# Optimization experiments

Hardware: AMD Instinct MI355X
Metric: run time of the kernel (lower is better)

## Reference

```python
import jax, jax.numpy as jnp
import numpy as np

HID = 512       # hidden_dim (embed/LSTM input)
HDE = 512       # hidden_dim_de == attn_channels (required by conv_att channel count)
NCLS = 7000
LSEQ = 40
B = 128
FH, FW = 8, 32


def setup_inputs() -> dict:
    key = jax.random.key(0)
    ks = jax.random.split(key, 16)
    s = 0.05
    inp = {
        "hidden_en": jax.random.normal(ks[0], (1, B, HID), jnp.float32),
        "x_em": jax.random.normal(ks[1], (B, HDE, FH, FW), jnp.float32),
        "att_x_em": jax.random.normal(ks[2], (B, FH * FW, HDE), jnp.float32),
        "target": jax.random.randint(ks[3], (B, LSEQ), 0, NCLS),
        "feature_h": FH,
        "feature_w": FW,
        # parameters
        "embed_w": jax.random.normal(ks[4], (NCLS, HID), jnp.float32) * s,
        "W_ih": jax.random.normal(ks[5], (4 * HDE, HID), jnp.float32) * s,   # LSTMCell input weights (i,f,g,o)
        "W_hh": jax.random.normal(ks[6], (4 * HDE, HDE), jnp.float32) * s,
        "b_ih": jax.random.normal(ks[7], (4 * HDE,), jnp.float32) * s,
        "b_hh": jax.random.normal(ks[8], (4 * HDE,), jnp.float32) * s,
        "hem_w": jax.random.normal(ks[9], (HDE, HDE), jnp.float32) * s,     # 1x1 conv h_em as matrix
        "hem_b": jax.random.normal(ks[10], (HDE,), jnp.float32) * s,
        "attw_w": jax.random.normal(ks[11], (HDE,), jnp.float32) * s,       # 1x1 conv conv_att -> 1 channel
        "attw_b": jax.random.normal(ks[12], (), jnp.float32) * s,
        "lin_w": jax.random.normal(ks[13], (NCLS, HDE + HDE), jnp.float32) * s,
        "lin_b": jax.random.normal(ks[14], (NCLS,), jnp.float32) * s,
    }
    return inp


def _decode(hidden_en, x_em, att_x_em, target, embed_w, W_ih, W_hh, b_ih, b_hh,
            hem_w, hem_b, attw_w, attw_b, lin_w, lin_b):
    L = target.shape[1]
    # teacher-forced inputs: step 0 uses hidden_en[-1], step t>=1 uses embed(target[:, t-1])
    xt0 = hidden_en[-1]                                   # [B, HID]
    xts = jnp.concatenate([xt0[None], jnp.transpose(embed_w[target[:, : L - 1]], (1, 0, 2))], axis=0)  # [L,B,HID]
    xg_all = jnp.einsum('lbi,gi->lbg', xts, W_ih) + b_ih  # precompute input gates [L,B,4H]
    Bn = x_em.shape[0]
    h0 = jnp.zeros((Bn, HDE), x_em.dtype)
    c0 = jnp.zeros((Bn, HDE), x_em.dtype)

    def step(carry, xg):
        h, c = carry
        gates = xg + h @ W_hh.T + b_hh
        i, f, g, o = jnp.split(gates, 4, axis=-1)
        c = jax.nn.sigmoid(f) * c + jax.nn.sigmoid(i) * jnp.tanh(g)
        h = jax.nn.sigmoid(o) * jnp.tanh(c)
        # additive attention (dropout treated as identity for determinism)
        hem = h @ hem_w.T + hem_b                          # [B, C]
        feat = jnp.tanh(x_em + hem[:, :, None, None])      # [B, C, H, W]
        feat_att = jnp.einsum('bchw,c->bhw', feat, attw_w) + attw_b
        alpha = jax.nn.softmax(feat_att.reshape(Bn, -1), axis=-1)  # [B, HW]
        att = jnp.einsum('bn,bnd->bd', alpha, att_x_em)    # [B, C]
        scores = jax.nn.log_softmax(jnp.concatenate([h, att], -1) @ lin_w.T + lin_b)
        return (h, c), scores

    _, ys = jax.lax.scan(step, (h0, c0), xg_all)           # ys: [L, B, NCLS]
    return jnp.transpose(ys, (1, 0, 2))                    # [B, L, NCLS]


def reference(hidden_en, x_em, att_x_em, target, feature_h, feature_w,
              embed_w, W_ih, W_hh, b_ih, b_hh, hem_w, hem_b, attw_w, attw_b,
              lin_w, lin_b):
    return _decode(hidden_en, x_em, att_x_em, target, embed_w, W_ih, W_hh,
                   b_ih, b_hh, hem_w, hem_b, attw_w, attw_b, lin_w, lin_b)
```

## Files before the change

kernel.cpp:

```cpp
#include <hip/hip_runtime.h>

#define B_    128
#define HIDD  512
#define NCLS  7000
#define NPAD  7040
#define LSEQ  40
#define MROWS 5120
#define TT    10
#define SBLK  16

typedef __attribute__((ext_vector_type(8))) short bf16x8;
typedef __attribute__((ext_vector_type(4))) float f32x4;

__device__ __forceinline__ unsigned short f2bf(float x) {
  union { float f; unsigned u; } v; v.f = x;
  unsigned r = v.u + 0x7fffu + ((v.u >> 16) & 1u);
  return (unsigned short)(r >> 16);
}
__device__ __forceinline__ float bf2f(unsigned short h) {
  union { unsigned u; float f; } v; v.u = ((unsigned)h) << 16;
  return v.f;
}
__device__ __forceinline__ float sigm(float x) { return 1.f / (1.f + __expf(-x)); }
__device__ __forceinline__ float tanh_f(float x) {
  float e = __expf(2.f * x);
  return 1.f - 2.f / (e + 1.f);
}
__device__ __forceinline__ float rcp_f(float x) { return __builtin_amdgcn_rcpf(x); }

__device__ __forceinline__ void gl_lds16(const void* g, void* l) {
  auto gp = reinterpret_cast<const __attribute__((address_space(1))) unsigned int*>(
      reinterpret_cast<unsigned long long>(g));
  auto lp = reinterpret_cast<__attribute__((address_space(3))) unsigned int*>(
      reinterpret_cast<unsigned long long>(l));
  __builtin_amdgcn_global_load_lds(gp, lp, 16, 0, 0);
}

__global__ __launch_bounds__(256) void k_cvt(const float* __restrict__ src,
                                             unsigned short* __restrict__ dst, int n4) {
  int i = blockIdx.x * 256 + threadIdx.x;
  if (i >= n4) return;
  float4 v = ((const float4*)src)[i];
  ushort4 o; o.x = f2bf(v.x); o.y = f2bf(v.y); o.z = f2bf(v.z); o.w = f2bf(v.w);
  ((ushort4*)dst)[i] = o;
}

__global__ __launch_bounds__(256) void k_cvtp(const float* __restrict__ src,
                                              unsigned short* __restrict__ dst,
                                              const float* __restrict__ b1,
                                              const float* __restrict__ b2,
                                              float* __restrict__ bsum) {
  int i = blockIdx.x * 256 + threadIdx.x;
  int e = i * 4;
  int n = e >> 9, col = e & 511;
  int srow = ((n >> 4) & 3) * 512 + (n >> 6) * 16 + (n & 15);
  float4 v = *(const float4*)(src + (size_t)srow * 512 + col);
  ushort4 o; o.x = f2bf(v.x); o.y = f2bf(v.y); o.z = f2bf(v.z); o.w = f2bf(v.w);
  ((ushort4*)dst)[i] = o;
  if (bsum != nullptr && col == 0) bsum[n] = b1[srow] + b2[srow];
}

__global__ __launch_bounds__(256) void k_expcvt(const float* __restrict__ src,
                                                unsigned short* __restrict__ dst, int n4) {
  int i = blockIdx.x * 256 + threadIdx.x;
  if (i >= n4) return;
  float4 v = ((const float4*)src)[i];
  ushort4 o;
  o.x = f2bf(__expf(2.f * v.x)); o.y = f2bf(__expf(2.f * v.y));
  o.z = f2bf(__expf(2.f * v.z)); o.w = f2bf(__expf(2.f * v.w));
  ((ushort4*)dst)[i] = o;
}

__global__ __launch_bounds__(256) void k_linpad(const float* __restrict__ lw,
                                                unsigned short* __restrict__ dst) {
  int i = blockIdx.x * 256 + threadIdx.x;
  int e = i * 4;
  int row = e >> 10;
  ushort4 o;
  if (row < NCLS) {
    float4 v = *(const float4*)(lw + (size_t)row * 1024 + (e & 1023));
    o.x = f2bf(v.x); o.y = f2bf(v.y); o.z = f2bf(v.z); o.w = f2bf(v.w);
  } else { o.x = 0; o.y = 0; o.z = 0; o.w = 0; }
  ((ushort4*)dst)[i] = o;
}

__global__ __launch_bounds__(256) void k_xts(const float* __restrict__ hidden_en,
                                             const float* __restrict__ embed_w,
                                             const int* __restrict__ target,
                                             unsigned short* __restrict__ xts,
                                             int* __restrict__ cnt) {
  if (blockIdx.x == 0 && threadIdx.x == 0)
    __hip_atomic_store(cnt, 0, __ATOMIC_RELAXED, __HIP_MEMORY_SCOPE_AGENT);
  int i = blockIdx.x * 256 + threadIdx.x;
  int e = i * 4;
  int r = e >> 9, col = e & 511;
  int l = r >> 7, b = r & 127;
  const float* src;
  if (l == 0) src = hidden_en + b * 512 + col;
  else        src = embed_w + (size_t)target[b * LSEQ + (l - 1)] * 512 + col;
  float4 v = *(const float4*)src;
  ushort4 o; o.x = f2bf(v.x); o.y = f2bf(v.y); o.z = f2bf(v.z); o.w = f2bf(v.w);
  ((ushort4*)xts)[i] = o;
}

template <int MODE>
__global__ __launch_bounds__(256) void k_gemm(const unsigned short* __restrict__ A, int lda,
                                              const unsigned short* __restrict__ Bw, int ldb,
                                              const float* __restrict__ bias,
                                              void* __restrict__ outp, int ldc, int K) {
  __shared__ __align__(16) unsigned short As[128 * 32];
  __shared__ __align__(16) unsigned short Bs[128 * 32];
  const int tid = threadIdx.x;
  const int lane = tid & 63, wid = tid >> 6;
  const int wm = wid >> 1, wn = wid & 1;
  const int quad = lane >> 4, l16 = lane & 15;
  const int gr = lane >> 2, gc = (lane & 3) * 8;
  const int m0 = blockIdx.x * 128, n0 = blockIdx.y * 128;
  f32x4 acc[4][4];
#pragma unroll
  for (int i = 0; i < 4; i++)
#pragma unroll
    for (int j = 0; j < 4; j++) acc[i][j] = (f32x4){0.f, 0.f, 0.f, 0.f};

  for (int k0 = 0; k0 < K; k0 += 32) {
#pragma unroll
    for (int s = 0; s < 2; s++) {
      const int rb = s * 64 + wid * 16;
      gl_lds16(A + (size_t)(m0 + rb + gr) * lda + k0 + gc, As + rb * 32);
      gl_lds16(Bw + (size_t)(n0 + rb + gr) * ldb + k0 + gc, Bs + rb * 32);
    }
    __syncthreads();
    bf16x8 af[4], bfr[4];
#pragma unroll
    for (int i = 0; i < 4; i++)
      af[i] = *(const bf16x8*)(As + (wm * 64 + i * 16 + l16) * 32 + quad * 8);
#pragma unroll
    for (int j = 0; j < 4; j++)
      bfr[j] = *(const bf16x8*)(Bs + (wn * 64 + j * 16 + l16) * 32 + quad * 8);
#pragma unroll
    for (int i = 0; i < 4; i++)
#pragma unroll
      for (int j = 0; j < 4; j++)
        acc[i][j] = __builtin_amdgcn_mfma_f32_16x16x32_bf16(af[i], bfr[j], acc[i][j], 0, 0, 0);
    __syncthreads();
  }
#pragma unroll
  for (int i = 0; i < 4; i++) {
    int mbase = m0 + wm * 64 + i * 16 + quad * 4;
#pragma unroll
    for (int j = 0; j < 4; j++) {
      int n = n0 + wn * 64 + j * 16 + l16;
#pragma unroll
      for (int r = 0; r < 4; r++) {
        float v = acc[i][j][r];
        int m = mbase + r;
        if (MODE == 0) {
          ((unsigned short*)outp)[(size_t)m * ldc + n] = f2bf(v + bias[n]);
        } else if (MODE == 3) {
          ((float*)outp)[(size_t)m * ldc + n] = __expf(2.f * (v + bias[n]));
        } else {
          if (n < NCLS) {
            int t = m >> 7, b = m & 127;
            ((float*)outp)[((size_t)(b * LSEQ + t)) * NCLS + n] = v + bias[n];
          }
        }
      }
    }
  }
}

__global__ __launch_bounds__(256) void k_step(const unsigned short* __restrict__ h_prev,
                                              unsigned short* __restrict__ h_new,
                                              float* __restrict__ c_buf,
                                              const unsigned short* __restrict__ xg,
                                              const unsigned short* __restrict__ whhp,
                                              unsigned short* __restrict__ hatt, int t) {
  __shared__ __align__(16) unsigned short As[128 * 32];
  __shared__ __align__(16) unsigned short Bs[128 * 32];
  const int tid = threadIdx.x;
  const int lane = tid & 63, wid = tid >> 6;
  const int wm = wid >> 1, wn = wid & 1;
  const int quad = lane >> 4, l16 = lane & 15;
  const int n0 = blockIdx.x * 128;
  f32x4 acc[4][4];
#pragma unroll
  for (int i = 0; i < 4; i++)
#pragma unroll
    for (int j = 0; j < 4; j++) acc[i][j] = (f32x4){0.f, 0.f, 0.f, 0.f};

  if (t > 0) {
    const int r0 = tid >> 2, kq0 = (tid & 3) * 8;
    for (int k0 = 0; k0 < 512; k0 += 32) {
#pragma unroll
      for (int s = 0; s < 2; s++) {
        int row = r0 + s * 64;
        *(bf16x8*)(As + row * 32 + kq0) = *(const bf16x8*)(h_prev + (size_t)row * 512 + k0 + kq0);
        *(bf16x8*)(Bs + row * 32 + kq0) = *(const bf16x8*)(whhp + (size_t)(n0 + row) * 512 + k0 + kq0);
      }
      __syncthreads();
      bf16x8 af[4], bfr[4];
#pragma unroll
      for (int i = 0; i < 4; i++)
        af[i] = *(const bf16x8*)(As + (wm * 64 + i * 16 + l16) * 32 + quad * 8);
#pragma unroll
      for (int j = 0; j < 4; j++)
        bfr[j] = *(const bf16x8*)(Bs + (wn * 64 + j * 16 + l16) * 32 + quad * 8);
#pragma unroll
      for (int i = 0; i < 4; i++)
#pragma unroll
        for (int j = 0; j < 4; j++)
          acc[i][j] = __builtin_amdgcn_mfma_f32_16x16x32_bf16(af[i], bfr[j], acc[i][j], 0, 0, 0);
      __syncthreads();
    }
  }
  const int jcol = ((n0 >> 6) + wn) * 16 + l16;
#pragma unroll
  for (int i = 0; i < 4; i++) {
    int mbase = wm * 64 + i * 16 + quad * 4;
#pragma unroll
    for (int r = 0; r < 4; r++) {
      int m = mbase + r;
      const unsigned short* xrow = xg + (size_t)(t * 128 + m) * 2048 + n0 + wn * 64 + l16;
      float ip = acc[i][0][r] + bf2f(xrow[0]);
      float fp = acc[i][1][r] + bf2f(xrow[16]);
      float gp = acc[i][2][r] + bf2f(xrow[32]);
      float op = acc[i][3][r] + bf2f(xrow[48]);
      float c_old = (t > 0) ? c_buf[m * 512 + jcol] : 0.f;
      float c = sigm(fp) * c_old + sigm(ip) * tanh_f(gp);
      c_buf[m * 512 + jcol] = c;
      float h = sigm(op) * tanh_f(c);
      unsigned short hb = f2bf(h);
      h_new[m * 512 + jcol] = hb;
      hatt[(size_t)(t * 128 + m) * 1024 + jcol] = hb;
    }
  }
}

__global__ __launch_bounds__(256) void k_scan3(unsigned short* __restrict__ h0,
                                               unsigned short* __restrict__ h1,
                                               const unsigned short* __restrict__ xg,
                                               const unsigned short* __restrict__ whhp,
                                               unsigned short* __restrict__ hatt,
                                               int* __restrict__ cnt) {
  __shared__ __align__(16) unsigned short Wl[128 * 512];
  const int tid = threadIdx.x;
  const int lane = tid & 63, wid = tid >> 6;
  const int wm = wid >> 1, wn = wid & 1;
  const int quad = lane >> 4, l16 = lane & 15;
  const int n0 = blockIdx.x * 128;

  for (int i = tid; i < 128 * 64; i += 256) {
    int row = i >> 6, c8 = (i & 63) << 3;
    bf16x8 v = *(const bf16x8*)(whhp + (size_t)(n0 + row) * 512 + c8);
    *(bf16x8*)((char*)Wl + ((row * 1024 + c8 * 2) ^ ((row & 7) << 4))) = v;
  }
  float cst[4][4];
#pragma unroll
  for (int i = 0; i < 4; i++)
#pragma unroll
    for (int r = 0; r < 4; r++) cst[i][r] = 0.f;
  const int jcol = ((n0 >> 6) + wn) * 16 + l16;
  __syncthreads();

  for (int t = 0; t < LSEQ; t++) {
    f32x4 acc[4][4];
#pragma unroll
    for (int i = 0; i < 4; i++)
#pragma unroll
      for (int j = 0; j < 4; j++) acc[i][j] = (f32x4){0.f, 0.f, 0.f, 0.f};
    if (t > 0) {
      const unsigned short* hp = (t & 1) ? h0 : h1;
      const unsigned short* hb = hp + (size_t)(wm * 64 + l16) * 512 + quad * 8;
#pragma unroll 4
      for (int k0 = 0; k0 < 512; k0 += 32) {
        bf16x8 af[4], bfr[4];
#pragma unroll
        for (int i = 0; i < 4; i++)
          af[i] = *(const bf16x8*)(hb + (size_t)i * 16 * 512 + k0);
#pragma unroll
        for (int j = 0; j < 4; j++) {
          int rw = wn * 64 + j * 16 + l16;
          bfr[j] = *(const bf16x8*)((const char*)Wl +
                    ((rw * 1024 + (k0 + quad * 8) * 2) ^ ((rw & 7) << 4)));
        }
#pragma unroll
        for (int i = 0; i < 4; i++)
#pragma unroll
          for (int j = 0; j < 4; j++)
            acc[i][j] = __builtin_amdgcn_mfma_f32_16x16x32_bf16(af[i], bfr[j], acc[i][j], 0, 0, 0);
      }
    }
    unsigned short* hn = (t & 1) ? h1 : h0;
    const unsigned short* xq = xg + (size_t)(t * 128) * 2048 + n0 + wn * 64 + l16;
#pragma unroll
    for (int i = 0; i < 4; i++) {
#pragma unroll
      for (int r = 0; r < 4; r++) {
        int m = wm * 64 + i * 16 + quad * 4 + r;
        const unsigned short* xrow = xq + (size_t)m * 2048;
        float ip = acc[i][0][r] + bf2f(xrow[0]);
        float fp = acc[i][1][r] + bf2f(xrow[16]);
        float gp = acc[i][2][r] + bf2f(xrow[32]);
        float op = acc[i][3][r] + bf2f(xrow[48]);
        float c = sigm(fp) * cst[i][r] + sigm(ip) * tanh_f(gp);
        cst[i][r] = c;
        float h = sigm(op) * tanh_f(c);
        unsigned short hbv = f2bf(h);
        hn[m * 512 + jcol] = hbv;
        hatt[(size_t)(t * 128 + m) * 1024 + jcol] = hbv;
      }
    }
    if (t < LSEQ - 1) {
      __threadfence();
      __syncthreads();
      if (tid == 0) {
        __hip_atomic_fetch_add(cnt, 1, __ATOMIC_RELEASE, __HIP_MEMORY_SCOPE_AGENT);
        const int tgt = SBLK * (t + 1);
        while (__hip_atomic_load(cnt, __ATOMIC_ACQUIRE, __HIP_MEMORY_SCOPE_AGENT) < tgt)
          __builtin_amdgcn_s_sleep(8);
      }
      __syncthreads();
      __threadfence();
    }
  }
}

__global__ __launch_bounds__(256) void k_feat(const float* __restrict__ Eh,
                                              const unsigned short* __restrict__ Ex,
                                              const float* __restrict__ attw_w,
                                              float* __restrict__ s_all) {
  __shared__ float EhL[TT][512];
  __shared__ float wL[512];
  const int tid = threadIdx.x;
  const int tg = blockIdx.x >> 7, b = blockIdx.x & 127;
  const int t0 = tg * TT;
  for (int i = tid * 4; i < TT * 512; i += 1024) {
    int t = i >> 9, c = i & 511;
    *(float4*)&EhL[t][c] = *(const float4*)&Eh[((size_t)(t0 + t) * 128 + b) * 512 + c];
  }
  if (tid < 128) *(float4*)&wL[tid * 4] = *(const float4*)&attw_w[tid * 4];
  __syncthreads();
  const int p = tid;
  const unsigned short* xp = Ex + (size_t)b * 512 * 256 + p;
  float acc[TT];
#pragma unroll
  for (int t = 0; t < TT; t++) acc[t] = 0.f;
  for (int c0 = 0; c0 < 512; c0 += 4) {
    float ex0 = bf2f(xp[(size_t)(c0 + 0) * 256]);
    float ex1 = bf2f(xp[(size_t)(c0 + 1) * 256]);
    float ex2 = bf2f(xp[(size_t)(c0 + 2) * 256]);
    float ex3 = bf2f(xp[(size_t)(c0 + 3) * 256]);
    float4 wv = *(const float4*)&wL[c0];
#pragma unroll
    for (int t = 0; t < TT; t++) {
      float4 eh = *(const float4*)&EhL[t][c0];
      acc[t] = __builtin_fmaf(wv.x, rcp_f(__builtin_fmaf(ex0, eh.x, 1.f)), acc[t]);
      acc[t] = __builtin_fmaf(wv.y, rcp_f(__builtin_fmaf(ex1, eh.y, 1.f)), acc[t]);
      acc[t] = __builtin_fmaf(wv.z, rcp_f(__builtin_fmaf(ex2, eh.z, 1.f)), acc[t]);
      acc[t] = __builtin_fmaf(wv.w, rcp_f(__builtin_fmaf(ex3, eh.w, 1.f)), acc[t]);
    }
  }
#pragma unroll
  for (int t = 0; t < TT; t++)
    s_all[((size_t)(t0 + t) * 128 + b) * 256 + p] = -2.f * acc[t];
}

__global__ __launch_bounds__(256) void k_att(const float* __restrict__ s_all,
                                             const float* __restrict__ atx,
                                             unsigned short* __restrict__ hatt) {
  __shared__ float sL[40][257];
  __shared__ float zinv[40];
  const int tid = threadIdx.x;
  const int b = blockIdx.x >> 1, dh = blockIdx.x & 1;
  for (int i = tid; i < 40 * 256; i += 256) {
    int t = i >> 8, p = i & 255;
    sL[t][p] = s_all[((size_t)t * 128 + b) * 256 + p];
  }
  __syncthreads();
  if (tid < 40) {
    int t = tid;
    float mx = -1e30f;
    for (int p = 0; p < 256; p++) mx = fmaxf(mx, sL[t][p]);
    float z = 0.f;
    for (int p = 0; p < 256; p++) { float e = __expf(sL[t][p] - mx); sL[t][p] = e; z += e; }
    zinv[t] = 1.f / z;
  }
  __syncthreads();
  float acc[40];
#pragma unroll
  for (int t = 0; t < 40; t++) acc[t] = 0.f;
  const int d = dh * 256 + tid;
  const float* ap = atx + (size_t)b * 256 * 512 + d;
  for (int p = 0; p < 256; p++) {
    float av = ap[(size_t)p * 512];
#pragma unroll
    for (int t = 0; t < 40; t++) acc[t] += sL[t][p] * av;
  }
#pragma unroll
  for (int t = 0; t < 40; t++) {
    float v = acc[t] * zinv[t];
    hatt[((size_t)t * 128 + b) * 1024 + 512 + d] = f2bf(v);
  }
}

__global__ __launch_bounds__(256) void k_lsm(float* __restrict__ out) {
  __shared__ float buf[7000];
  __shared__ float red[256];
  const int tid = threadIdx.x;
  float* pr = out + (size_t)blockIdx.x * NCLS;
  for (int i = tid * 4; i < NCLS; i += 1024)
    *(float4*)&buf[i] = *(const float4*)&pr[i];
  __syncthreads();
  float mx = -1e30f;
  for (int i = tid; i < NCLS; i += 256) mx = fmaxf(mx, buf[i]);
  red[tid] = mx; __syncthreads();
  for (int s = 128; s > 0; s >>= 1) { if (tid < s) red[tid] = fmaxf(red[tid], red[tid + s]); __syncthreads(); }
  mx = red[0]; __syncthreads();
  float sum = 0.f;
  for (int i = tid; i < NCLS; i += 256) sum += __expf(buf[i] - mx);
  red[tid] = sum; __syncthreads();
  for (int s = 128; s > 0; s >>= 1) { if (tid < s) red[tid] += red[tid + s]; __syncthreads(); }
  float lse = mx + __logf(red[0]);
  for (int i = tid * 4; i < NCLS; i += 1024) {
    float4 v = *(const float4*)&buf[i];
    v.x -= lse; v.y -= lse; v.z -= lse; v.w -= lse;
    *(float4*)&pr[i] = v;
  }
}

extern "C" void kernel_launch(void* const* d_in, const int* in_sizes, int n_in,
                              void* d_out, int out_size, void* d_ws, size_t ws_size,
                              hipStream_t stream) {
  const float* hidden_en = (const float*)d_in[0];
  const float* x_em      = (const float*)d_in[1];
  const float* att_x     = (const float*)d_in[2];
  const int*   target    = (const int*)d_in[3];
  const float* embed_w   = (const float*)d_in[6];
  const float* W_ih      = (const float*)d_in[7];
  const float* W_hh      = (const float*)d_in[8];
  const float* b_ih      = (const float*)d_in[9];
  const float* b_hh      = (const float*)d_in[10];
  const float* hem_w     = (const float*)d_in[11];
  const float* hem_b     = (const float*)d_in[12];
  const float* attw_w    = (const float*)d_in[13];
  const float* lin_w     = (const float*)d_in[15];
  const float* lin_b     = (const float*)d_in[16];
  float* out = (float*)d_out;
  (void)in_sizes; (void)n_in; (void)out_size; (void)ws_size;

  char* w = (char*)d_ws;
  size_t off = 0;
  auto alloc = [&](size_t bytes) { char* p = w + off; off = (off + bytes + 255) & ~(size_t)255; return p; };
  unsigned short* xts  = (unsigned short*)alloc((size_t)MROWS * 512 * 2);
  unsigned short* wihp = (unsigned short*)alloc((size_t)2048 * 512 * 2);
  unsigned short* whhp = (unsigned short*)alloc((size_t)2048 * 512 * 2);
  unsigned short* xg   = (unsigned short*)alloc((size_t)MROWS * 2048 * 2);
  unsigned short* hemw = (unsigned short*)alloc((size_t)512 * 512 * 2);
  unsigned short* linw = (unsigned short*)alloc((size_t)NPAD * 1024 * 2);
  unsigned short* xem  = (unsigned short*)alloc((size_t)128 * 512 * 256 * 2);
  unsigned short* hatt = (unsigned short*)alloc((size_t)MROWS * 1024 * 2);
  unsigned short* h0   = (unsigned short*)alloc((size_t)128 * 512 * 2);
  unsigned short* h1   = (unsigned short*)alloc((size_t)128 * 512 * 2);
  float* cb      = (float*)alloc((size_t)128 * 512 * 4);
  float* bsum    = (float*)alloc((size_t)2048 * 4);
  float* eh_all  = (float*)alloc((size_t)MROWS * 512 * 4);
  float* s_all   = (float*)alloc((size_t)MROWS * 256 * 4);
  int*   cnt     = (int*)alloc(256);

  k_cvtp<<<1024, 256, 0, stream>>>(W_ih, wihp, b_ih, b_hh, bsum);
  k_cvtp<<<1024, 256, 0, stream>>>(W_hh, whhp, nullptr, nullptr, nullptr);
  k_cvt<<<256, 256, 0, stream>>>(hem_w, hemw, 512 * 512 / 4);
  k_expcvt<<<16384, 256, 0, stream>>>(x_em, xem, 128 * 512 * 256 / 4);
  k_linpad<<<NPAD * 1024 / 4 / 256, 256, 0, stream>>>(lin_w, linw);
  k_xts<<<MROWS * 512 / 4 / 256, 256, 0, stream>>>(hidden_en, embed_w, target, xts, cnt);
  k_gemm<0><<<dim3(40, 16), 256, 0, stream>>>(xts, 512, wihp, 512, bsum, xg, 2048, 512);

  {
    void* args[] = { (void*)&h0, (void*)&h1, (void*)&xg, (void*)&whhp, (void*)&hatt, (void*)&cnt };
    hipError_t ce = hipLaunchCooperativeKernel(k_scan3, dim3(SBLK), dim3(256), args, 0u, stream);
    if (ce != hipSuccess) {
      for (int t = 0; t < LSEQ; t++) {
        const unsigned short* hp = (t & 1) ? h0 : h1;
        unsigned short* hn = (t & 1) ? h1 : h0;
        k_step<<<16, 256, 0, stream>>>(hp, hn, cb, xg, whhp, hatt, t);
      }
    }
  }

  k_gemm<3><<<dim3(40, 4), 256, 0, stream>>>(hatt, 1024, hemw, 512, hem_b, eh_all, 512, 512);
  k_feat<<<512, 256, 0, stream>>>(eh_all, xem, attw_w, s_all);
  k_att<<<256, 256, 0, stream>>>(s_all, att_x, hatt);

  k_gemm<2><<<dim3(40, 55), 256, 0, stream>>>(hatt, 1024, linw, 1024, lin_b, out, NCLS, 1024);
  k_lsm<<<MROWS, 256, 0, stream>>>(out);
}
```

Baseline: 1.408 ms.

## Fuse preprocessing kernels, relax scan barrier fences, use plain LDS staging in GEMM

Merges six conversion and gather kernels into one launch, which removes several kernel-launch gaps. In the cooperative LSTM scan, the hidden state is now written with cache-bypassing stores and read with nontemporal loads. The thread fences and acquire/release atomics around the grid barrier become relaxed atomics with a shorter sleep, cutting per-step sync cost. The GEMM drops direct global-to-LDS loads in favour of ordinary register-staged copies. Relaxing the memory ordering risks stale h reads if the cache-bypass assumptions do not hold.

```diff
diff --git a/kernel.cpp b/kernel.cpp
--- a/kernel.cpp
+++ b/kernel.cpp
@@ -28,79 +28,73 @@
 }
 __device__ __forceinline__ float rcp_f(float x) { return __builtin_amdgcn_rcpf(x); }
 
-__device__ __forceinline__ void gl_lds16(const void* g, void* l) {
-  auto gp = reinterpret_cast<const __attribute__((address_space(1))) unsigned int*>(
-      reinterpret_cast<unsigned long long>(g));
-  auto lp = reinterpret_cast<__attribute__((address_space(3))) unsigned int*>(
-      reinterpret_cast<unsigned long long>(l));
-  __builtin_amdgcn_global_load_lds(gp, lp, 16, 0, 0);
-}
-
-__global__ __launch_bounds__(256) void k_cvt(const float* __restrict__ src,
-                                             unsigned short* __restrict__ dst, int n4) {
-  int i = blockIdx.x * 256 + threadIdx.x;
-  if (i >= n4) return;
-  float4 v = ((const float4*)src)[i];
-  ushort4 o; o.x = f2bf(v.x); o.y = f2bf(v.y); o.z = f2bf(v.z); o.w = f2bf(v.w);
-  ((ushort4*)dst)[i] = o;
-}
-
-__global__ __launch_bounds__(256) void k_cvtp(const float* __restrict__ src,
-                                              unsigned short* __restrict__ dst,
-                                              const float* __restrict__ b1,
-                                              const float* __restrict__ b2,
-                                              float* __restrict__ bsum) {
-  int i = blockIdx.x * 256 + threadIdx.x;
-  int e = i * 4;
-  int n = e >> 9, col = e & 511;
-  int srow = ((n >> 4) & 3) * 512 + (n >> 6) * 16 + (n & 15);
-  float4 v = *(const float4*)(src + (size_t)srow * 512 + col);
-  ushort4 o; o.x = f2bf(v.x); o.y = f2bf(v.y); o.z = f2bf(v.z); o.w = f2bf(v.w);
-  ((ushort4*)dst)[i] = o;
-  if (bsum != nullptr && col == 0) bsum[n] = b1[srow] + b2[srow];
-}
-
-__global__ __launch_bounds__(256) void k_expcvt(const float* __restrict__ src,
-                                                unsigned short* __restrict__ dst, int n4) {
-  int i = blockIdx.x * 256 + threadIdx.x;
-  if (i >= n4) return;
-  float4 v = ((const float4*)src)[i];
-  ushort4 o;
-  o.x = f2bf(__expf(2.f * v.x)); o.y = f2bf(__expf(2.f * v.y));
-  o.z = f2bf(__expf(2.f * v.z)); o.w = f2bf(__expf(2.f * v.w));
-  ((ushort4*)dst)[i] = o;
-}
-
-__global__ __launch_bounds__(256) void k_linpad(const float* __restrict__ lw,
-                                                unsigned short* __restrict__ dst) {
-  int i = blockIdx.x * 256 + threadIdx.x;
-  int e = i * 4;
-  int row = e >> 10;
-  ushort4 o;
-  if (row < NCLS) {
-    float4 v = *(const float4*)(lw + (size_t)row * 1024 + (e & 1023));
-    o.x = f2bf(v.x); o.y = f2bf(v.y); o.z = f2bf(v.z); o.w = f2bf(v.w);
-  } else { o.x = 0; o.y = 0; o.z = 0; o.w = 0; }
-  ((ushort4*)dst)[i] = o;
-}
-
-__global__ __launch_bounds__(256) void k_xts(const float* __restrict__ hidden_en,
+__global__ __launch_bounds__(256) void k_pre(const float* __restrict__ W_ih,
+                                             const float* __restrict__ W_hh,
+                                             unsigned short* __restrict__ wihp,
+                                             unsigned short* __restrict__ whhp,
+                                             const float* __restrict__ b_ih,
+                                             const float* __restrict__ b_hh,
+                                             float* __restrict__ bsum,
+                                             const float* __restrict__ hem_w,
+                                             unsigned short* __restrict__ hemw,
+                                             const float* __restrict__ x_em,
+                                             unsigned short* __restrict__ xem,
+                                             const float* __restrict__ lin_w,
+                                             unsigned short* __restrict__ linw,
+                                             const float* __restrict__ hidden_en,
                                              const float* __restrict__ embed_w,
                                              const int* __restrict__ target,
                                              unsigned short* __restrict__ xts,
                                              int* __restrict__ cnt) {
-  if (blockIdx.x == 0 && threadIdx.x == 0)
+  const int bid = blockIdx.x, tid = threadIdx.x;
+  if (bid == 0 && tid == 0)
     __hip_atomic_store(cnt, 0, __ATOMIC_RELAXED, __HIP_MEMORY_SCOPE_AGENT);
-  int i = blockIdx.x * 256 + threadIdx.x;
-  int e = i * 4;
-  int r = e >> 9, col = e & 511;
-  int l = r >> 7, b = r & 127;
-  const float* src;
-  if (l == 0) src = hidden_en + b * 512 + col;
-  else        src = embed_w + (size_t)target[b * LSEQ + (l - 1)] * 512 + col;
-  float4 v = *(const float4*)src;
-  ushort4 o; o.x = f2bf(v.x); o.y = f2bf(v.y); o.z = f2bf(v.z); o.w = f2bf(v.w);
-  ((ushort4*)xts)[i] = o;
+  if (bid < 2048) {
+    const bool isA = bid < 1024;
+    const float* src = isA ? W_ih : W_hh;
+    unsigned short* dst = isA ? wihp : whhp;
+    int i = (isA ? bid : bid - 1024) * 256 + tid;
+    int e = i * 4;
+    int n = e >> 9, col = e & 511;
+    int srow = ((n >> 4) & 3) * 512 + (n >> 6) * 16 + (n & 15);
+    float4 v = *(const float4*)(src + (size_t)srow * 512 + col);
+    ushort4 o; o.x = f2bf(v.x); o.y = f2bf(v.y); o.z = f2bf(v.z); o.w = f2bf(v.w);
+    ((ushort4*)dst)[i] = o;
+    if (isA && col == 0) bsum[n] = b_ih[srow] + b_hh[srow];
+  } else if (bid < 2304) {
+    int i = (bid - 2048) * 256 + tid;
+    float4 v = ((const float4*)hem_w)[i];
+    ushort4 o; o.x = f2bf(v.x); o.y = f2bf(v.y); o.z = f2bf(v.z); o.w = f2bf(v.w);
+    ((ushort4*)hemw)[i] = o;
+  } else if (bid < 18688) {
+    int i = (bid - 2304) * 256 + tid;
+    float4 v = ((const float4*)x_em)[i];
+    ushort4 o;
+    o.x = f2bf(__expf(2.f * v.x)); o.y = f2bf(__expf(2.f * v.y));
+    o.z = f2bf(__expf(2.f * v.z)); o.w = f2bf(__expf(2.f * v.w));
+    ((ushort4*)xem)[i] = o;
+  } else if (bid < 25728) {
+    int i = (bid - 18688) * 256 + tid;
+    int e = i * 4;
+    int row = e >> 10;
+    ushort4 o;
+    if (row < NCLS) {
+      float4 v = *(const float4*)(lin_w + (size_t)row * 1024 + (e & 1023));
+      o.x = f2bf(v.x); o.y = f2bf(v.y); o.z = f2bf(v.z); o.w = f2bf(v.w);
+    } else { o.x = 0; o.y = 0; o.z = 0; o.w = 0; }
+    ((ushort4*)linw)[i] = o;
+  } else {
+    int i = (bid - 25728) * 256 + tid;
+    int e = i * 4;
+    int r = e >> 9, col = e & 511;
+    int l = r >> 7, b = r & 127;
+    const float* src;
+    if (l == 0) src = hidden_en + b * 512 + col;
+    else        src = embed_w + (size_t)target[b * LSEQ + (l - 1)] * 512 + col;
+    float4 v = *(const float4*)src;
+    ushort4 o; o.x = f2bf(v.x); o.y = f2bf(v.y); o.z = f2bf(v.z); o.w = f2bf(v.w);
+    ((ushort4*)xts)[i] = o;
+  }
 }
 
 template <int MODE>
@@ -114,7 +108,6 @@
   const int lane = tid & 63, wid = tid >> 6;
   const int wm = wid >> 1, wn = wid & 1;
   const int quad = lane >> 4, l16 = lane & 15;
-  const int gr = lane >> 2, gc = (lane & 3) * 8;
   const int m0 = blockIdx.x * 128, n0 = blockIdx.y * 128;
   f32x4 acc[4][4];
 #pragma unroll
@@ -122,12 +115,13 @@
 #pragma unroll
     for (int j = 0; j < 4; j++) acc[i][j] = (f32x4){0.f, 0.f, 0.f, 0.f};
 
+  const int r0 = tid >> 2, kq0 = (tid & 3) * 8;
   for (int k0 = 0; k0 < K; k0 += 32) {
 #pragma unroll
     for (int s = 0; s < 2; s++) {
-      const int rb = s * 64 + wid * 16;
-      gl_lds16(A + (size_t)(m0 + rb + gr) * lda + k0 + gc, As + rb * 32);
-      gl_lds16(Bw + (size_t)(n0 + rb + gr) * ldb + k0 + gc, Bs + rb * 32);
+      int row = r0 + s * 64;
+      *(bf16x8*)(As + row * 32 + kq0) = *(const bf16x8*)(A + (size_t)(m0 + row) * lda + k0 + kq0);
+      *(bf16x8*)(Bs + row * 32 + kq0) = *(const bf16x8*)(Bw + (size_t)(n0 + row) * ldb + k0 + kq0);
     }
     __syncthreads();
     bf16x8 af[4], bfr[4];
@@ -236,7 +230,7 @@
   }
 }
 
-__global__ __launch_bounds__(256) void k_scan3(unsigned short* __restrict__ h0,
+__global__ __launch_bounds__(256) void k_scan4(unsigned short* __restrict__ h0,
                                                unsigned short* __restrict__ h1,
                                                const unsigned short* __restrict__ xg,
                                                const unsigned short* __restrict__ whhp,
@@ -276,7 +270,8 @@
         bf16x8 af[4], bfr[4];
 #pragma unroll
         for (int i = 0; i < 4; i++)
-          af[i] = *(const bf16x8*)(hb + (size_t)i * 16 * 512 + k0);
+          af[i] = __builtin_nontemporal_load(
+              (const bf16x8*)(hb + (size_t)i * 16 * 512 + k0));
 #pragma unroll
         for (int j = 0; j < 4; j++) {
           int rw = wn * 64 + j * 16 + l16;
@@ -306,21 +301,22 @@
         cst[i][r] = c;
         float h = sigm(op) * tanh_f(c);
         unsigned short hbv = f2bf(h);
-        hn[m * 512 + jcol] = hbv;
+        unsigned short* hdst = hn + m * 512 + jcol;
+        asm volatile("global_store_short %0, %1, off sc0 sc1"
+                     :: "v"(hdst), "v"((unsigned)hbv) : "memory");
         hatt[(size_t)(t * 128 + m) * 1024 + jcol] = hbv;
       }
     }
     if (t < LSEQ - 1) {
-      __threadfence();
       __syncthreads();
       if (tid == 0) {
-        __hip_atomic_fetch_add(cnt, 1, __ATOMIC_RELEASE, __HIP_MEMORY_SCOPE_AGENT);
+        __hip_atomic_fetch_add(cnt, 1, __ATOMIC_RELAXED, __HIP_MEMORY_SCOPE_AGENT);
         const int tgt = SBLK * (t + 1);
-        while (__hip_atomic_load(cnt, __ATOMIC_ACQUIRE, __HIP_MEMORY_SCOPE_AGENT) < tgt)
-          __builtin_amdgcn_s_sleep(8);
+        while (__hip_atomic_fetch_add(cnt, 0, __ATOMIC_RELAXED,
+                                      __HIP_MEMORY_SCOPE_AGENT) < tgt)
+          __builtin_amdgcn_s_sleep(4);
       }
       __syncthreads();
-      __threadfence();
     }
   }
 }
@@ -467,17 +463,14 @@
   float* s_all   = (float*)alloc((size_t)MROWS * 256 * 4);
   int*   cnt     = (int*)alloc(256);
 
-  k_cvtp<<<1024, 256, 0, stream>>>(W_ih, wihp, b_ih, b_hh, bsum);
-  k_cvtp<<<1024, 256, 0, stream>>>(W_hh, whhp, nullptr, nullptr, nullptr);
-  k_cvt<<<256, 256, 0, stream>>>(hem_w, hemw, 512 * 512 / 4);
-  k_expcvt<<<16384, 256, 0, stream>>>(x_em, xem, 128 * 512 * 256 / 4);
-  k_linpad<<<NPAD * 1024 / 4 / 256, 256, 0, stream>>>(lin_w, linw);
-  k_xts<<<MROWS * 512 / 4 / 256, 256, 0, stream>>>(hidden_en, embed_w, target, xts, cnt);
+  k_pre<<<28288, 256, 0, stream>>>(W_ih, W_hh, wihp, whhp, b_ih, b_hh, bsum,
+                                   hem_w, hemw, x_em, xem, lin_w, linw,
+                                   hidden_en, embed_w, target, xts, cnt);
   k_gemm<0><<<dim3(40, 16), 256, 0, stream>>>(xts, 512, wihp, 512, bsum, xg, 2048, 512);
 
   {
     void* args[] = { (void*)&h0, (void*)&h1, (void*)&xg, (void*)&whhp, (void*)&hatt, (void*)&cnt };
-    hipError_t ce = hipLaunchCooperativeKernel(k_scan3, dim3(SBLK), dim3(256), args, 0u, stream);
+    hipError_t ce = hipLaunchCooperativeKernel(k_scan4, dim3(SBLK), dim3(256), args, 0u, stream);
     if (ce != hipSuccess) {
       for (int t = 0; t < LSEQ; t++) {
         const unsigned short* hp = (t & 1) ? h0 : h1;
```

Measured after the change: 1.794 ms. 27.4% more time.
